# Kernel optimization log

Hardware: AMD Instinct MI355X
Metric: run time of the kernel (lower is better)

The kernel has to match this reference:

```python
import jax, jax.numpy as jnp
import numpy as np

N_IN, N_HIDDEN, N, K = 14, 256, 131072, 10

def _linear_params(key, n_in, n_out):
    kw, kb = jax.random.split(key)
    lim = 1.0 / np.sqrt(n_in)
    W = jax.random.uniform(kw, (n_in, n_out), jnp.float32, -lim, lim)
    b = jax.random.uniform(kb, (n_out,), jnp.float32, -lim, lim)
    return W, b

def setup_inputs() -> dict:
    key = jax.random.key(0)
    ks = jax.random.split(key, 8)
    towers = jax.random.normal(ks[0], (N, K, N_IN), jnp.float32)
    M1_w, M1_b = _linear_params(ks[1], N_IN + N_HIDDEN, N_HIDDEN)
    M2_w, M2_b = _linear_params(ks[2], N_HIDDEN, N_HIDDEN)
    M3_w, M3_b = _linear_params(ks[3], N_HIDDEN, N_HIDDEN)
    O1_w, O1_b = _linear_params(ks[4], N_IN + N_HIDDEN, N_HIDDEN)
    O2_w, O2_b = _linear_params(ks[5], N_HIDDEN, N_HIDDEN)
    O3_w, O3_b = _linear_params(ks[6], N_HIDDEN, 1)
    aggregate = jnp.zeros((1, N_HIDDEN), jnp.float32)
    return dict(towers=towers, aggregate=aggregate,
                M1_w=M1_w, M1_b=M1_b, M2_w=M2_w, M2_b=M2_b, M3_w=M3_w, M3_b=M3_b,
                O1_w=O1_w, O1_b=O1_b, O2_w=O2_w, O2_b=O2_b, O3_w=O3_w, O3_b=O3_b,
                k=K)

def reference(towers, aggregate,
              M1_w, M1_b, M2_w, M2_b, M3_w, M3_b,
              O1_w, O1_b, O2_w, O2_b, O3_w, O3_b, k):
    N_, K_, _ = towers.shape
    # flip along tower axis, then scan over K steps (top-down)
    tows = jnp.transpose(towers[:, ::-1, :], (1, 0, 2))  # (K, N, n_in)

    def mlp_M(x):
        h = jax.nn.relu(x @ M1_w + M1_b)
        h = jax.nn.relu(h @ M2_w + M2_b)
        return jax.nn.relu(h @ M3_w + M3_b)

    def mlp_O(x):
        h = jax.nn.relu(x @ O1_w + O1_b)
        h = jax.nn.relu(h @ O2_w + O2_b)
        return h @ O3_w + O3_b  # (N, 1)

    def step(carry, tow_k):
        summary, prod = carry
        x = jnp.concatenate([summary, tow_k], axis=1)  # (N, n_hidden + n_in)
        pred = jax.nn.sigmoid(mlp_O(x))[:, 0]
        new_summary = mlp_M(x)
        return (new_summary, prod * pred), None

    init_summary = jnp.broadcast_to(aggregate, (N_, aggregate.shape[1]))
    init_prod = jnp.ones((N_,), towers.dtype)
    (final_summary, prod), _ = jax.lax.scan(step, (init_summary, init_prod), tows)
    return prod  # (N,)
```

## Files before the change

### kernel.cpp

```cpp
#include <hip/hip_runtime.h>
#include <math.h>
#include <stdint.h>


typedef _Float16 half8 __attribute__((ext_vector_type(8)));
typedef __fp16 fp16x2 __attribute__((ext_vector_type(2)));
typedef float f32x4 __attribute__((ext_vector_type(4)));

constexpr int KS = 10;
constexpr int RSTR = 584;
constexpr float SPLIT_S = 2048.f;
constexpr float SPLIT_INV = 1.f / 2048.f;

__device__ __align__(16) _Float16 g_Wh[672 * 512];
__device__ __align__(16) _Float16 g_Wl[672 * 512];
__device__ __align__(16) uint4 g_park[2048u * 8u * 8u * 64u];

__global__ void prep_w(const float* __restrict__ O1w, const float* __restrict__ M1w,
                       const float* __restrict__ O2w, const float* __restrict__ M2w,
                       const float* __restrict__ M3w) {
  const int bid = blockIdx.x, l = threadIdx.x;
  const float* W; int Ksrc, f;
  if (bid < 144)      { W = O1w; Ksrc = 270; f = bid; }
  else if (bid < 288) { W = M1w; Ksrc = 270; f = bid - 144; }
  else if (bid < 416) { W = O2w; Ksrc = 256; f = bid - 288; }
  else if (bid < 544) { W = M2w; Ksrc = 256; f = bid - 416; }
  else                { W = M3w; Ksrc = 256; f = bid - 544; }
  const int c = f >> 4, nt = f & 15, g = l >> 4, s = l & 15;
  const int of = nt * 16 + s;
  union { half8 h; uint4 u; } hv, lv;
#pragma unroll
  for (int i = 0; i < 8; ++i) {
    const int k = c * 32 + g * 8 + i;
    const float w = (k < Ksrc) ? W[k * 256 + of] : 0.f;
    const _Float16 h = (_Float16)w;
    hv.h[i] = h;
    lv.h[i] = (_Float16)((w - (float)h) * SPLIT_S);
  }
  ((uint4*)g_Wh)[bid * 64 + l] = hv.u;
  ((uint4*)g_Wl)[bid * 64 + l] = lv.u;
}

__device__ __forceinline__ half8 as_half8(uint4 u) {
  union { uint4 u4; half8 h; } c; c.u4 = u; return c.h;
}
__device__ __forceinline__ f32x4 mfma16(half8 a, half8 b, f32x4 c) {
  return __builtin_amdgcn_mfma_f32_16x16x32_f16(a, b, c, 0, 0, 0);
}
__device__ __forceinline__ uint32_t h2bits(fp16x2 h) {
  union { fp16x2 h2; uint32_t u; } c; c.h2 = h; return c.u;
}

struct PK { uint2 hi, lo; };
__device__ __forceinline__ PK split4(float v0, float v1, float v2, float v3) {
  fp16x2 h01 = __builtin_amdgcn_cvt_pkrtz(v0, v1);
  fp16x2 h23 = __builtin_amdgcn_cvt_pkrtz(v2, v3);
  fp16x2 l01 = __builtin_amdgcn_cvt_pkrtz((v0 - (float)h01[0]) * SPLIT_S,
                                          (v1 - (float)h01[1]) * SPLIT_S);
  fp16x2 l23 = __builtin_amdgcn_cvt_pkrtz((v2 - (float)h23[0]) * SPLIT_S,
                                          (v3 - (float)h23[1]) * SPLIT_S);
  PK r;
  r.hi = make_uint2(h2bits(h01), h2bits(h23));
  r.lo = make_uint2(h2bits(l01), h2bits(l23));
  return r;
}
__device__ __forceinline__ void split1(float v, _Float16& h, _Float16& l) {
  h = (_Float16)v;
  l = (_Float16)((v - (float)h) * SPLIT_S);
}

__device__ __forceinline__ void zero24(f32x4 a1[2][4], f32x4 a2[2][4]) {
#pragma unroll
  for (int n = 0; n < 2; ++n)
#pragma unroll
    for (int sf = 0; sf < 4; ++sf) {
      a1[n][sf] = (f32x4){0.f, 0.f, 0.f, 0.f};
      a2[n][sf] = (f32x4){0.f, 0.f, 0.f, 0.f};
    }
}

template <int CHUNKS>
__device__ __forceinline__ void lgemm(f32x4 a1[2][4], f32x4 a2[2][4],
                                      const _Float16* __restrict__ Xs,
                                      const uint4* __restrict__ Wh,
                                      const uint4* __restrict__ Wl,
                                      int wu, int g, int s) {
#pragma unroll 1
  for (int c = 0; c < CHUNKS; ++c) {
    uint4 wh[2], wl[2];
#pragma unroll
    for (int n = 0; n < 2; ++n) {
      wh[n] = Wh[(c * 16 + 2 * wu + n) * 64];
      wl[n] = Wl[(c * 16 + 2 * wu + n) * 64];
    }
#pragma unroll
    for (int sf = 0; sf < 4; ++sf) {
      const _Float16* xp = Xs + (16 * sf + s) * RSTR + c * 32 + g * 8;
      half8 bh = *(const half8*)xp;
      half8 bl = *(const half8*)(xp + 288);
#pragma unroll
      for (int n = 0; n < 2; ++n) {
        a1[n][sf] = mfma16(as_half8(wh[n]), bh, a1[n][sf]);
        a2[n][sf] = mfma16(as_half8(wh[n]), bl, a2[n][sf]);
        a2[n][sf] = mfma16(as_half8(wl[n]), bh, a2[n][sf]);
      }
    }
  }
}

__device__ __forceinline__ void epi_write(const f32x4 a1[2][4], const f32x4 a2[2][4],
                                          const float* __restrict__ bias,
                                          _Float16* __restrict__ Xs,
                                          int wu, int g, int s) {
#pragma unroll
  for (int n = 0; n < 2; ++n) {
    const float4 bv = *(const float4*)(bias + (2 * wu + n) * 16 + 4 * g);
#pragma unroll
    for (int sf = 0; sf < 4; ++sf) {
      const float v0 = fmaxf(fmaf(a2[n][sf][0], SPLIT_INV, a1[n][sf][0]) + bv.x, 0.f);
      const float v1 = fmaxf(fmaf(a2[n][sf][1], SPLIT_INV, a1[n][sf][1]) + bv.y, 0.f);
      const float v2 = fmaxf(fmaf(a2[n][sf][2], SPLIT_INV, a1[n][sf][2]) + bv.z, 0.f);
      const float v3 = fmaxf(fmaf(a2[n][sf][3], SPLIT_INV, a1[n][sf][3]) + bv.w, 0.f);
      const PK p = split4(v0, v1, v2, v3);
      _Float16* yp = Xs + (16 * sf + s) * RSTR + (2 * wu + n) * 16 + 4 * g;
      *(uint2*)yp = p.hi;
      *(uint2*)(yp + 288) = p.lo;
    }
  }
}

__device__ __forceinline__ void epi_park(const f32x4 a1[2][4], const f32x4 a2[2][4],
                                         const float* __restrict__ bias,
                                         uint4* __restrict__ slot,
                                         int wu, int g, int l) {
#pragma unroll
  for (int n = 0; n < 2; ++n) {
    const float4 bv = *(const float4*)(bias + (2 * wu + n) * 16 + 4 * g);
#pragma unroll
    for (int p = 0; p < 2; ++p) {
      PK q[2];
#pragma unroll
      for (int h = 0; h < 2; ++h) {
        const int sf = 2 * p + h;
        const float v0 = fmaxf(fmaf(a2[n][sf][0], SPLIT_INV, a1[n][sf][0]) + bv.x, 0.f);
        const float v1 = fmaxf(fmaf(a2[n][sf][1], SPLIT_INV, a1[n][sf][1]) + bv.y, 0.f);
        const float v2 = fmaxf(fmaf(a2[n][sf][2], SPLIT_INV, a1[n][sf][2]) + bv.z, 0.f);
        const float v3 = fmaxf(fmaf(a2[n][sf][3], SPLIT_INV, a1[n][sf][3]) + bv.w, 0.f);
        q[h] = split4(v0, v1, v2, v3);
      }
      slot[(n * 2 + p) * 64 + l]     = make_uint4(q[0].hi.x, q[0].hi.y, q[1].hi.x, q[1].hi.y);
      slot[(4 + n * 2 + p) * 64 + l] = make_uint4(q[0].lo.x, q[0].lo.y, q[1].lo.x, q[1].lo.y);
    }
  }
}

__device__ __forceinline__ void unpark_write(const uint4 pk[8],
                                             _Float16* __restrict__ Xs,
                                             int wu, int g, int s) {
#pragma unroll
  for (int n = 0; n < 2; ++n)
#pragma unroll
    for (int p = 0; p < 2; ++p) {
      const uint4 hi = pk[n * 2 + p];
      const uint4 lo = pk[4 + n * 2 + p];
#pragma unroll
      for (int h = 0; h < 2; ++h) {
        const int sf = 2 * p + h;
        _Float16* yp = Xs + (16 * sf + s) * RSTR + (2 * wu + n) * 16 + 4 * g;
        *(uint2*)yp = h ? make_uint2(hi.z, hi.w) : make_uint2(hi.x, hi.y);
        *(uint2*)(yp + 288) = h ? make_uint2(lo.z, lo.w) : make_uint2(lo.x, lo.y);
      }
    }
}

__global__ __launch_bounds__(512, 4) void topdown_mfma(
    const float* __restrict__ towers, const float* __restrict__ aggregate,
    const float* __restrict__ O1b, const float* __restrict__ O2b,
    const float* __restrict__ O3w, const float* __restrict__ O3b,
    const float* __restrict__ M1b, const float* __restrict__ M2b,
    const float* __restrict__ M3b, float* __restrict__ out) {
  __shared__ __align__(16) _Float16 Xs[64 * RSTR];
  __shared__ __align__(16) float scr[64][8];
  const int t = threadIdx.x, l = t & 63;
  const int wu = __builtin_amdgcn_readfirstlane(t >> 6);
  const int g = l >> 4, s = l & 15;
  const int n0 = blockIdx.x * 64;
  uint4* park = g_park + ((size_t)blockIdx.x * 8 + (size_t)wu) * (8 * 64);

  for (int idx = t; idx < 64 * 288; idx += 512) {
    const int ss = idx / 288, f = idx - ss * 288;
    const float v = (f < 256) ? aggregate[f] : 0.f;
    _Float16 h, lo; split1(v, h, lo);
    Xs[ss * RSTR + f] = h;
    Xs[ss * RSTR + 288 + f] = lo;
  }

  float prod = 1.f;
  const float o3bias = O3b[0];
  f32x4 a1[2][4], a2[2][4];

  const uint4* WhL = (const uint4*)g_Wh + l;
  const uint4* WlL = (const uint4*)g_Wl + l;

  for (int kk = 0; kk < KS; ++kk) {
    const int tbase = (KS - 1 - kk) * 14;
    for (int idx = t; idx < 64 * 14; idx += 512) {
      const int ss = idx / 14, f = idx - ss * 14;
      const float v = towers[(size_t)(n0 + ss) * (KS * 14) + tbase + f];
      _Float16 h, lo; split1(v, h, lo);
      Xs[ss * RSTR + 256 + f] = h;
      Xs[ss * RSTR + 288 + 256 + f] = lo;
    }
    __syncthreads();

    zero24(a1, a2);
    lgemm<9>(a1, a2, Xs, WhL + 144 * 64, WlL + 144 * 64, wu, g, s);
    epi_park(a1, a2, M1b, park, wu, g, l);

    zero24(a1, a2);
    lgemm<9>(a1, a2, Xs, WhL, WlL, wu, g, s);
    __syncthreads();
    epi_write(a1, a2, O1b, Xs, wu, g, s);
    __syncthreads();

    zero24(a1, a2);
    lgemm<8>(a1, a2, Xs, WhL + 288 * 64, WlL + 288 * 64, wu, g, s);

    asm volatile("" ::: "memory");
    uint4 pk[8];
#pragma unroll
    for (int q = 0; q < 8; ++q) pk[q] = park[q * 64 + l];

    float tp[4] = {0.f, 0.f, 0.f, 0.f};
#pragma unroll
    for (int n = 0; n < 2; ++n) {
      const int ob = (2 * wu + n) * 16 + 4 * g;
      const float4 bv = *(const float4*)(O2b + ob);
      const float4 ov = *(const float4*)(O3w + ob);
      const float bb[4] = {bv.x, bv.y, bv.z, bv.w};
      const float oo[4] = {ov.x, ov.y, ov.z, ov.w};
#pragma unroll
      for (int sf = 0; sf < 4; ++sf)
#pragma unroll
        for (int r = 0; r < 4; ++r)
          tp[sf] += fmaxf(fmaf(a2[n][sf][r], SPLIT_INV, a1[n][sf][r]) + bb[r], 0.f) * oo[r];
    }
#pragma unroll
    for (int sf = 0; sf < 4; ++sf) {
      tp[sf] += __shfl_xor(tp[sf], 16);
      tp[sf] += __shfl_xor(tp[sf], 32);
    }
    if (g == 0) {
#pragma unroll
      for (int sf = 0; sf < 4; ++sf) scr[16 * sf + s][wu] = tp[sf];
    }
    __syncthreads();

    unpark_write(pk, Xs, wu, g, s);
    if (t < 64) {
      const float4 s0 = *(const float4*)(scr[t]);
      const float4 s1 = *(const float4*)(scr[t] + 4);
      const float tt = ((s0.x + s0.y) + (s0.z + s0.w)) +
                       ((s1.x + s1.y) + (s1.z + s1.w)) + o3bias;
      prod *= 1.f / (1.f + expf(-tt));
    }
    __syncthreads();

    zero24(a1, a2);
    lgemm<8>(a1, a2, Xs, WhL + 416 * 64, WlL + 416 * 64, wu, g, s);
    __syncthreads();
    epi_write(a1, a2, M2b, Xs, wu, g, s);
    __syncthreads();

    zero24(a1, a2);
    lgemm<8>(a1, a2, Xs, WhL + 544 * 64, WlL + 544 * 64, wu, g, s);
    __syncthreads();
    epi_write(a1, a2, M3b, Xs, wu, g, s);
  }

  if (t < 64) out[n0 + t] = prod;
}

extern "C" void kernel_launch(void* const* d_in, const int* in_sizes, int n_in,
                              void* d_out, int out_size, void* d_ws, size_t ws_size,
                              hipStream_t stream) {
  const float* towers    = (const float*)d_in[0];
  const float* aggregate = (const float*)d_in[1];
  const float* M1w = (const float*)d_in[2];
  const float* M1b = (const float*)d_in[3];
  const float* M2w = (const float*)d_in[4];
  const float* M2b = (const float*)d_in[5];
  const float* M3w = (const float*)d_in[6];
  const float* M3b = (const float*)d_in[7];
  const float* O1w = (const float*)d_in[8];
  const float* O1b = (const float*)d_in[9];
  const float* O2w = (const float*)d_in[10];
  const float* O2b = (const float*)d_in[11];
  const float* O3w = (const float*)d_in[12];
  const float* O3b = (const float*)d_in[13];
  float* out = (float*)d_out;

  prep_w<<<672, 64, 0, stream>>>(O1w, M1w, O2w, M2w, M3w);

  const int nblocks = out_size / 64;
  topdown_mfma<<<nblocks, 512, 0, stream>>>(towers, aggregate, O1b, O2b, O3w,
                                            O3b, M1b, M2b, M3b, out);
}
```

Before: 2.408 ms.

## Retile warp work to 4 output tiles by 2 sample tiles

Each wave's GEMM tile changes from 2 output-column fragments by 4 sample fragments to 4 output-column fragments by 2 sample fragments, splitting the 8 waves into 4 column groups and 2 sample groups. Each wave now loads twice as many weight fragments from global/L2 per chunk but half as many activation fragments from LDS. The O3 reduction scratch shrinks to 4 partials per sample. The intent is to cut LDS read traffic per MFMA, at the cost of doubling the per-wave weight fetches from global memory.

After: 2.853 ms. +18.5%, slower.

```diff
diff --git a/kernel.cpp b/kernel.cpp
--- a/kernel.cpp
+++ b/kernel.cpp
@@ -69,37 +69,38 @@
   l = (_Float16)((v - (float)h) * SPLIT_S);
 }
 
-__device__ __forceinline__ void zero24(f32x4 a1[2][4], f32x4 a2[2][4]) {
-#pragma unroll
-  for (int n = 0; n < 2; ++n)
-#pragma unroll
-    for (int sf = 0; sf < 4; ++sf) {
+__device__ __forceinline__ void zero42(f32x4 a1[4][2], f32x4 a2[4][2]) {
+#pragma unroll
+  for (int n = 0; n < 4; ++n)
+#pragma unroll
+    for (int sf = 0; sf < 2; ++sf) {
       a1[n][sf] = (f32x4){0.f, 0.f, 0.f, 0.f};
       a2[n][sf] = (f32x4){0.f, 0.f, 0.f, 0.f};
     }
 }
 
 template <int CHUNKS>
-__device__ __forceinline__ void lgemm(f32x4 a1[2][4], f32x4 a2[2][4],
+__device__ __forceinline__ void lgemm(f32x4 a1[4][2], f32x4 a2[4][2],
                                       const _Float16* __restrict__ Xs,
                                       const uint4* __restrict__ Wh,
                                       const uint4* __restrict__ Wl,
-                                      int wu, int g, int s) {
+                                      int wn, int sg, int g, int s) {
 #pragma unroll 1
   for (int c = 0; c < CHUNKS; ++c) {
-    uint4 wh[2], wl[2];
-#pragma unroll
-    for (int n = 0; n < 2; ++n) {
-      wh[n] = Wh[(c * 16 + 2 * wu + n) * 64];
-      wl[n] = Wl[(c * 16 + 2 * wu + n) * 64];
-    }
-#pragma unroll
-    for (int sf = 0; sf < 4; ++sf) {
-      const _Float16* xp = Xs + (16 * sf + s) * RSTR + c * 32 + g * 8;
+    uint4 wh[4], wl[4];
+#pragma unroll
+    for (int n = 0; n < 4; ++n) {
+      wh[n] = Wh[(c * 16 + 4 * wn + n) * 64];
+      wl[n] = Wl[(c * 16 + 4 * wn + n) * 64];
+    }
+#pragma unroll
+    for (int sf = 0; sf < 2; ++sf) {
+      const _Float16* xp =
+          Xs + (16 * (2 * sg + sf) + s) * RSTR + c * 32 + g * 8;
       half8 bh = *(const half8*)xp;
       half8 bl = *(const half8*)(xp + 288);
 #pragma unroll
-      for (int n = 0; n < 2; ++n) {
+      for (int n = 0; n < 4; ++n) {
         a1[n][sf] = mfma16(as_half8(wh[n]), bh, a1[n][sf]);
         a2[n][sf] = mfma16(as_half8(wh[n]), bl, a2[n][sf]);
         a2[n][sf] = mfma16(as_half8(wl[n]), bh, a2[n][sf]);
@@ -108,69 +109,64 @@
   }
 }
 
-__device__ __forceinline__ void epi_write(const f32x4 a1[2][4], const f32x4 a2[2][4],
+__device__ __forceinline__ void epi_write(const f32x4 a1[4][2], const f32x4 a2[4][2],
                                           const float* __restrict__ bias,
                                           _Float16* __restrict__ Xs,
-                                          int wu, int g, int s) {
-#pragma unroll
-  for (int n = 0; n < 2; ++n) {
-    const float4 bv = *(const float4*)(bias + (2 * wu + n) * 16 + 4 * g);
-#pragma unroll
-    for (int sf = 0; sf < 4; ++sf) {
+                                          int wn, int sg, int g, int s) {
+#pragma unroll
+  for (int n = 0; n < 4; ++n) {
+    const float4 bv = *(const float4*)(bias + (4 * wn + n) * 16 + 4 * g);
+#pragma unroll
+    for (int sf = 0; sf < 2; ++sf) {
       const float v0 = fmaxf(fmaf(a2[n][sf][0], SPLIT_INV, a1[n][sf][0]) + bv.x, 0.f);
       const float v1 = fmaxf(fmaf(a2[n][sf][1], SPLIT_INV, a1[n][sf][1]) + bv.y, 0.f);
       const float v2 = fmaxf(fmaf(a2[n][sf][2], SPLIT_INV, a1[n][sf][2]) + bv.z, 0.f);
       const float v3 = fmaxf(fmaf(a2[n][sf][3], SPLIT_INV, a1[n][sf][3]) + bv.w, 0.f);
       const PK p = split4(v0, v1, v2, v3);
-      _Float16* yp = Xs + (16 * sf + s) * RSTR + (2 * wu + n) * 16 + 4 * g;
+      _Float16* yp =
+          Xs + (16 * (2 * sg + sf) + s) * RSTR + (4 * wn + n) * 16 + 4 * g;
       *(uint2*)yp = p.hi;
       *(uint2*)(yp + 288) = p.lo;
     }
   }
 }
 
-__device__ __forceinline__ void epi_park(const f32x4 a1[2][4], const f32x4 a2[2][4],
+__device__ __forceinline__ void epi_park(const f32x4 a1[4][2], const f32x4 a2[4][2],
                                          const float* __restrict__ bias,
                                          uint4* __restrict__ slot,
-                                         int wu, int g, int l) {
-#pragma unroll
-  for (int n = 0; n < 2; ++n) {
-    const float4 bv = *(const float4*)(bias + (2 * wu + n) * 16 + 4 * g);
-#pragma unroll
-    for (int p = 0; p < 2; ++p) {
-      PK q[2];
-#pragma unroll
-      for (int h = 0; h < 2; ++h) {
-        const int sf = 2 * p + h;
-        const float v0 = fmaxf(fmaf(a2[n][sf][0], SPLIT_INV, a1[n][sf][0]) + bv.x, 0.f);
-        const float v1 = fmaxf(fmaf(a2[n][sf][1], SPLIT_INV, a1[n][sf][1]) + bv.y, 0.f);
-        const float v2 = fmaxf(fmaf(a2[n][sf][2], SPLIT_INV, a1[n][sf][2]) + bv.z, 0.f);
-        const float v3 = fmaxf(fmaf(a2[n][sf][3], SPLIT_INV, a1[n][sf][3]) + bv.w, 0.f);
-        q[h] = split4(v0, v1, v2, v3);
-      }
-      slot[(n * 2 + p) * 64 + l]     = make_uint4(q[0].hi.x, q[0].hi.y, q[1].hi.x, q[1].hi.y);
-      slot[(4 + n * 2 + p) * 64 + l] = make_uint4(q[0].lo.x, q[0].lo.y, q[1].lo.x, q[1].lo.y);
-    }
+                                         int wn, int g, int l) {
+#pragma unroll
+  for (int n = 0; n < 4; ++n) {
+    const float4 bv = *(const float4*)(bias + (4 * wn + n) * 16 + 4 * g);
+    PK q[2];
+#pragma unroll
+    for (int sf = 0; sf < 2; ++sf) {
+      const float v0 = fmaxf(fmaf(a2[n][sf][0], SPLIT_INV, a1[n][sf][0]) + bv.x, 0.f);
+      const float v1 = fmaxf(fmaf(a2[n][sf][1], SPLIT_INV, a1[n][sf][1]) + bv.y, 0.f);
+      const float v2 = fmaxf(fmaf(a2[n][sf][2], SPLIT_INV, a1[n][sf][2]) + bv.z, 0.f);
+      const float v3 = fmaxf(fmaf(a2[n][sf][3], SPLIT_INV, a1[n][sf][3]) + bv.w, 0.f);
+      q[sf] = split4(v0, v1, v2, v3);
+    }
+    slot[n * 64 + l]       = make_uint4(q[0].hi.x, q[0].hi.y, q[1].hi.x, q[1].hi.y);
+    slot[(4 + n) * 64 + l] = make_uint4(q[0].lo.x, q[0].lo.y, q[1].lo.x, q[1].lo.y);
   }
 }
 
 __device__ __forceinline__ void unpark_write(const uint4 pk[8],
                                              _Float16* __restrict__ Xs,
-                                             int wu, int g, int s) {
-#pragma unroll
-  for (int n = 0; n < 2; ++n)
-#pragma unroll
-    for (int p = 0; p < 2; ++p) {
-      const uint4 hi = pk[n * 2 + p];
-      const uint4 lo = pk[4 + n * 2 + p];
-#pragma unroll
-      for (int h = 0; h < 2; ++h) {
-        const int sf = 2 * p + h;
-        _Float16* yp = Xs + (16 * sf + s) * RSTR + (2 * wu + n) * 16 + 4 * g;
-        *(uint2*)yp = h ? make_uint2(hi.z, hi.w) : make_uint2(hi.x, hi.y);
-        *(uint2*)(yp + 288) = h ? make_uint2(lo.z, lo.w) : make_uint2(lo.x, lo.y);
-      }
-    }
+                                             int wn, int sg, int g, int s) {
+#pragma unroll
+  for (int n = 0; n < 4; ++n) {
+    const uint4 hi = pk[n];
+    const uint4 lo = pk[4 + n];
+#pragma unroll
+    for (int sf = 0; sf < 2; ++sf) {
+      _Float16* yp =
+          Xs + (16 * (2 * sg + sf) + s) * RSTR + (4 * wn + n) * 16 + 4 * g;
+      *(uint2*)yp = sf ? make_uint2(hi.z, hi.w) : make_uint2(hi.x, hi.y);
+      *(uint2*)(yp + 288) = sf ? make_uint2(lo.z, lo.w) : make_uint2(lo.x, lo.y);
+    }
+  }
 }
 
 __global__ __launch_bounds__(512, 4) void topdown_mfma(
@@ -180,9 +176,11 @@
     const float* __restrict__ M1b, const float* __restrict__ M2b,
     const float* __restrict__ M3b, float* __restrict__ out) {
   __shared__ __align__(16) _Float16 Xs[64 * RSTR];
-  __shared__ __align__(16) float scr[64][8];
+  __shared__ __align__(16) float scr[64][4];
   const int t = threadIdx.x, l = t & 63;
   const int wu = __builtin_amdgcn_readfirstlane(t >> 6);
+  const int wn = wu & 3;
+  const int sg = wu >> 2;
   const int g = l >> 4, s = l & 15;
   const int n0 = blockIdx.x * 64;
   uint4* park = g_park + ((size_t)blockIdx.x * 8 + (size_t)wu) * (8 * 64);
@@ -197,7 +195,7 @@
 
   float prod = 1.f;
   const float o3bias = O3b[0];
-  f32x4 a1[2][4], a2[2][4];
+  f32x4 a1[4][2], a2[4][2];
 
   const uint4* WhL = (const uint4*)g_Wh + l;
   const uint4* WlL = (const uint4*)g_Wl + l;
@@ -213,69 +211,66 @@
     }
     __syncthreads();
 
-    zero24(a1, a2);
-    lgemm<9>(a1, a2, Xs, WhL + 144 * 64, WlL + 144 * 64, wu, g, s);
-    epi_park(a1, a2, M1b, park, wu, g, l);
-
-    zero24(a1, a2);
-    lgemm<9>(a1, a2, Xs, WhL, WlL, wu, g, s);
-    __syncthreads();
-    epi_write(a1, a2, O1b, Xs, wu, g, s);
-    __syncthreads();
-
-    zero24(a1, a2);
-    lgemm<8>(a1, a2, Xs, WhL + 288 * 64, WlL + 288 * 64, wu, g, s);
+    zero42(a1, a2);
+    lgemm<9>(a1, a2, Xs, WhL + 144 * 64, WlL + 144 * 64, wn, sg, g, s);
+    epi_park(a1, a2, M1b, park, wn, g, l);
+
+    zero42(a1, a2);
+    lgemm<9>(a1, a2, Xs, WhL, WlL, wn, sg, g, s);
+    __syncthreads();
+    epi_write(a1, a2, O1b, Xs, wn, sg, g, s);
+    __syncthreads();
+
+    zero42(a1, a2);
+    lgemm<8>(a1, a2, Xs, WhL + 288 * 64, WlL + 288 * 64, wn, sg, g, s);
 
     asm volatile("" ::: "memory");
     uint4 pk[8];
 #pragma unroll
     for (int q = 0; q < 8; ++q) pk[q] = park[q * 64 + l];
 
-    float tp[4] = {0.f, 0.f, 0.f, 0.f};
-#pragma unroll
-    for (int n = 0; n < 2; ++n) {
-      const int ob = (2 * wu + n) * 16 + 4 * g;
+    float tp[2] = {0.f, 0.f};
+#pragma unroll
+    for (int n = 0; n < 4; ++n) {
+      const int ob = (4 * wn + n) * 16 + 4 * g;
       const float4 bv = *(const float4*)(O2b + ob);
       const float4 ov = *(const float4*)(O3w + ob);
       const float bb[4] = {bv.x, bv.y, bv.z, bv.w};
       const float oo[4] = {ov.x, ov.y, ov.z, ov.w};
 #pragma unroll
-      for (int sf = 0; sf < 4; ++sf)
+      for (int sf = 0; sf < 2; ++sf)
 #pragma unroll
         for (int r = 0; r < 4; ++r)
           tp[sf] += fmaxf(fmaf(a2[n][sf][r], SPLIT_INV, a1[n][sf][r]) + bb[r], 0.f) * oo[r];
     }
 #pragma unroll
-    for (int sf = 0; sf < 4; ++sf) {
+    for (int sf = 0; sf < 2; ++sf) {
       tp[sf] += __shfl_xor(tp[sf], 16);
       tp[sf] += __shfl_xor(tp[sf], 32);
     }
     if (g == 0) {
 #pragma unroll
-      for (int sf = 0; sf < 4; ++sf) scr[16 * sf + s][wu] = tp[sf];
-    }
-    __syncthreads();
-
-    unpark_write(pk, Xs, wu, g, s);
+      for (int sf = 0; sf < 2; ++sf) scr[16 * (2 * sg + sf) + s][wn] = tp[sf];
+    }
+    __syncthreads();
+
+    unpark_write(pk, Xs, wn, sg, g, s);
     if (t < 64) {
-      const float4 s0 = *(const float4*)(scr[t]);
-      const float4 s1 = *(const float4*)(scr[t] + 4);
-      const float tt = ((s0.x + s0.y) + (s0.z + s0.w)) +
-                       ((s1.x + s1.y) + (s1.z + s1.w)) + o3bias;
-      prod *= 1.f / (1.f + expf(-tt));
-    }
-    __syncthreads();
-
-    zero24(a1, a2);
-    lgemm<8>(a1, a2, Xs, WhL + 416 * 64, WlL + 416 * 64, wu, g, s);
-    __syncthreads();
-    epi_write(a1, a2, M2b, Xs, wu, g, s);
-    __syncthreads();
-
-    zero24(a1, a2);
-    lgemm<8>(a1, a2, Xs, WhL + 544 * 64, WlL + 544 * 64, wu, g, s);
-    __syncthreads();
-    epi_write(a1, a2, M3b, Xs, wu, g, s);
+      const float4 sv = *(const float4*)(scr[t]);
+      prod *= 1.f / (1.f + expf(-(sv.x + sv.y + sv.z + sv.w + o3bias)));
+    }
+    __syncthreads();
+
+    zero42(a1, a2);
+    lgemm<8>(a1, a2, Xs, WhL + 416 * 64, WlL + 416 * 64, wn, sg, g, s);
+    __syncthreads();
+    epi_write(a1, a2, M2b, Xs, wn, sg, g, s);
+    __syncthreads();
+
+    zero42(a1, a2);
+    lgemm<8>(a1, a2, Xs, WhL + 544 * 64, WlL + 544 * 64, wn, sg, g, s);
+    __syncthreads();
+    epi_write(a1, a2, M3b, Xs, wn, sg, g, s);
   }
 
   if (t < 64) out[n0 + t] = prod;
```

## Switch split-fp16 GEMMs from 16x16x32 to 32x32x16 MFMA with weight prefetch

Applied to the files above, without the earlier changes.

Replaces the 16x16x32 MFMA tiling with 32x32x16 MFMA tiles, so each wave computes 32 output features by 64 samples in two 16-wide accumulators. The weight prep layout, epilogues, parking and the O3 reduction are rewritten to match the new accumulator layout. The GEMM loop also double-buffers weight loads across chunks. The aim is fewer LDS reads of X per MFMA and better MFMA throughput, at the cost of larger accumulator register use, which risks occupancy under the 512x4 launch bounds.

Measured after the change: 3.078 ms. 27.8% more time.

```diff
diff --git a/kernel.cpp b/kernel.cpp
--- a/kernel.cpp
+++ b/kernel.cpp
@@ -5,7 +5,7 @@
 
 typedef _Float16 half8 __attribute__((ext_vector_type(8)));
 typedef __fp16 fp16x2 __attribute__((ext_vector_type(2)));
-typedef float f32x4 __attribute__((ext_vector_type(4)));
+typedef float f32x16 __attribute__((ext_vector_type(16)));
 
 constexpr int KS = 10;
 constexpr int RSTR = 584;
@@ -26,12 +26,13 @@
   else if (bid < 416) { W = O2w; Ksrc = 256; f = bid - 288; }
   else if (bid < 544) { W = M2w; Ksrc = 256; f = bid - 416; }
   else                { W = M3w; Ksrc = 256; f = bid - 544; }
-  const int c = f >> 4, nt = f & 15, g = l >> 4, s = l & 15;
-  const int of = nt * 16 + s;
+  const int kc = f >> 3, ot = f & 7;
+  const int of = ot * 32 + (l & 31);
+  const int kb = kc * 16 + (l >> 5) * 8;
   union { half8 h; uint4 u; } hv, lv;
 #pragma unroll
   for (int i = 0; i < 8; ++i) {
-    const int k = c * 32 + g * 8 + i;
+    const int k = kb + i;
     const float w = (k < Ksrc) ? W[k * 256 + of] : 0.f;
     const _Float16 h = (_Float16)w;
     hv.h[i] = h;
@@ -44,8 +45,8 @@
 __device__ __forceinline__ half8 as_half8(uint4 u) {
   union { uint4 u4; half8 h; } c; c.u4 = u; return c.h;
 }
-__device__ __forceinline__ f32x4 mfma16(half8 a, half8 b, f32x4 c) {
-  return __builtin_amdgcn_mfma_f32_16x16x32_f16(a, b, c, 0, 0, 0);
+__device__ __forceinline__ f32x16 mfma32(half8 a, half8 b, f32x16 c) {
+  return __builtin_amdgcn_mfma_f32_32x32x16_f16(a, b, c, 0, 0, 0);
 }
 __device__ __forceinline__ uint32_t h2bits(fp16x2 h) {
   union { fp16x2 h2; uint32_t u; } c; c.h2 = h; return c.u;
@@ -69,108 +70,129 @@
   l = (_Float16)((v - (float)h) * SPLIT_S);
 }
 
-__device__ __forceinline__ void zero24(f32x4 a1[2][4], f32x4 a2[2][4]) {
-#pragma unroll
-  for (int n = 0; n < 2; ++n)
-#pragma unroll
-    for (int sf = 0; sf < 4; ++sf) {
-      a1[n][sf] = (f32x4){0.f, 0.f, 0.f, 0.f};
-      a2[n][sf] = (f32x4){0.f, 0.f, 0.f, 0.f};
-    }
+struct W4 { uint4 h0, l0, h1, l1; };
+__device__ __forceinline__ W4 ldw(const uint4* __restrict__ Wh,
+                                  const uint4* __restrict__ Wl, int fb) {
+  W4 w;
+  w.h0 = Wh[fb * 64];
+  w.l0 = Wl[fb * 64];
+  w.h1 = Wh[(fb + 8) * 64];
+  w.l1 = Wl[(fb + 8) * 64];
+  return w;
+}
+
+__device__ __forceinline__ void body32(f32x16& a10, f32x16& a11,
+                                       f32x16& a20, f32x16& a21,
+                                       const _Float16* __restrict__ Xp0,
+                                       const _Float16* __restrict__ Xp1,
+                                       int coff, const W4& w) {
+#pragma unroll
+  for (int kk = 0; kk < 2; ++kk) {
+    const half8 wh = as_half8(kk ? w.h1 : w.h0);
+    const half8 wl = as_half8(kk ? w.l1 : w.l0);
+    const int o = coff + kk * 16;
+    half8 bh0 = *(const half8*)(Xp0 + o);
+    half8 bl0 = *(const half8*)(Xp0 + o + 288);
+    a10 = mfma32(wh, bh0, a10);
+    a20 = mfma32(wh, bl0, a20);
+    a20 = mfma32(wl, bh0, a20);
+    half8 bh1 = *(const half8*)(Xp1 + o);
+    half8 bl1 = *(const half8*)(Xp1 + o + 288);
+    a11 = mfma32(wh, bh1, a11);
+    a21 = mfma32(wh, bl1, a21);
+    a21 = mfma32(wl, bh1, a21);
+  }
 }
 
 template <int CHUNKS>
-__device__ __forceinline__ void lgemm(f32x4 a1[2][4], f32x4 a2[2][4],
-                                      const _Float16* __restrict__ Xs,
-                                      const uint4* __restrict__ Wh,
-                                      const uint4* __restrict__ Wl,
-                                      int wu, int g, int s) {
+__device__ __forceinline__ void lgemm32(f32x16& a10, f32x16& a11,
+                                        f32x16& a20, f32x16& a21,
+                                        const _Float16* __restrict__ Xp0,
+                                        const _Float16* __restrict__ Xp1,
+                                        const uint4* __restrict__ Wh,
+                                        const uint4* __restrict__ Wl, int wu) {
+  W4 A = ldw(Wh, Wl, wu);
+  W4 B;
 #pragma unroll 1
-  for (int c = 0; c < CHUNKS; ++c) {
-    uint4 wh[2], wl[2];
-#pragma unroll
-    for (int n = 0; n < 2; ++n) {
-      wh[n] = Wh[(c * 16 + 2 * wu + n) * 64];
-      wl[n] = Wl[(c * 16 + 2 * wu + n) * 64];
-    }
-#pragma unroll
-    for (int sf = 0; sf < 4; ++sf) {
-      const _Float16* xp = Xs + (16 * sf + s) * RSTR + c * 32 + g * 8;
-      half8 bh = *(const half8*)xp;
-      half8 bl = *(const half8*)(xp + 288);
-#pragma unroll
-      for (int n = 0; n < 2; ++n) {
-        a1[n][sf] = mfma16(as_half8(wh[n]), bh, a1[n][sf]);
-        a2[n][sf] = mfma16(as_half8(wh[n]), bl, a2[n][sf]);
-        a2[n][sf] = mfma16(as_half8(wl[n]), bh, a2[n][sf]);
-      }
-    }
-  }
-}
-
-__device__ __forceinline__ void epi_write(const f32x4 a1[2][4], const f32x4 a2[2][4],
+  for (int c = 0; c + 2 <= CHUNKS; c += 2) {
+    B = ldw(Wh, Wl, 16 * (c + 1) + wu);
+    body32(a10, a11, a20, a21, Xp0, Xp1, c * 32, A);
+    if (c + 2 < CHUNKS) A = ldw(Wh, Wl, 16 * (c + 2) + wu);
+    body32(a10, a11, a20, a21, Xp0, Xp1, (c + 1) * 32, B);
+  }
+  if (CHUNKS & 1) body32(a10, a11, a20, a21, Xp0, Xp1, (CHUNKS - 1) * 32, A);
+}
+
+__device__ __forceinline__ void zero2(f32x16& a, f32x16& b) {
+#pragma unroll
+  for (int i = 0; i < 16; ++i) { a[i] = 0.f; b[i] = 0.f; }
+}
+
+__device__ __forceinline__ void epi_write(const f32x16 a1[2], const f32x16 a2[2],
                                           const float* __restrict__ bias,
                                           _Float16* __restrict__ Xs,
-                                          int wu, int g, int s) {
-#pragma unroll
-  for (int n = 0; n < 2; ++n) {
-    const float4 bv = *(const float4*)(bias + (2 * wu + n) * 16 + 4 * g);
-#pragma unroll
-    for (int sf = 0; sf < 4; ++sf) {
-      const float v0 = fmaxf(fmaf(a2[n][sf][0], SPLIT_INV, a1[n][sf][0]) + bv.x, 0.f);
-      const float v1 = fmaxf(fmaf(a2[n][sf][1], SPLIT_INV, a1[n][sf][1]) + bv.y, 0.f);
-      const float v2 = fmaxf(fmaf(a2[n][sf][2], SPLIT_INV, a1[n][sf][2]) + bv.z, 0.f);
-      const float v3 = fmaxf(fmaf(a2[n][sf][3], SPLIT_INV, a1[n][sf][3]) + bv.w, 0.f);
+                                          int wu, int col, int hi) {
+#pragma unroll
+  for (int sf = 0; sf < 2; ++sf) {
+    _Float16* yrow = Xs + (32 * sf + col) * RSTR;
+#pragma unroll
+    for (int q = 0; q < 4; ++q) {
+      const int ofb = 32 * wu + 8 * q + 4 * hi;
+      const float4 bv = *(const float4*)(bias + ofb);
+      const float v0 = fmaxf(fmaf(a2[sf][4*q+0], SPLIT_INV, a1[sf][4*q+0]) + bv.x, 0.f);
+      const float v1 = fmaxf(fmaf(a2[sf][4*q+1], SPLIT_INV, a1[sf][4*q+1]) + bv.y, 0.f);
+      const float v2 = fmaxf(fmaf(a2[sf][4*q+2], SPLIT_INV, a1[sf][4*q+2]) + bv.z, 0.f);
+      const float v3 = fmaxf(fmaf(a2[sf][4*q+3], SPLIT_INV, a1[sf][4*q+3]) + bv.w, 0.f);
       const PK p = split4(v0, v1, v2, v3);
-      _Float16* yp = Xs + (16 * sf + s) * RSTR + (2 * wu + n) * 16 + 4 * g;
-      *(uint2*)yp = p.hi;
-      *(uint2*)(yp + 288) = p.lo;
-    }
-  }
-}
-
-__device__ __forceinline__ void epi_park(const f32x4 a1[2][4], const f32x4 a2[2][4],
+      *(uint2*)(yrow + ofb) = p.hi;
+      *(uint2*)(yrow + 288 + ofb) = p.lo;
+    }
+  }
+}
+
+__device__ __forceinline__ void epi_park(const f32x16 a1[2], const f32x16 a2[2],
                                          const float* __restrict__ bias,
                                          uint4* __restrict__ slot,
-                                         int wu, int g, int l) {
-#pragma unroll
-  for (int n = 0; n < 2; ++n) {
-    const float4 bv = *(const float4*)(bias + (2 * wu + n) * 16 + 4 * g);
-#pragma unroll
-    for (int p = 0; p < 2; ++p) {
-      PK q[2];
+                                         int wu, int hi, int l) {
+#pragma unroll
+  for (int sf = 0; sf < 2; ++sf)
+#pragma unroll
+    for (int qq = 0; qq < 2; ++qq) {
+      PK p[2];
 #pragma unroll
       for (int h = 0; h < 2; ++h) {
-        const int sf = 2 * p + h;
-        const float v0 = fmaxf(fmaf(a2[n][sf][0], SPLIT_INV, a1[n][sf][0]) + bv.x, 0.f);
-        const float v1 = fmaxf(fmaf(a2[n][sf][1], SPLIT_INV, a1[n][sf][1]) + bv.y, 0.f);
-        const float v2 = fmaxf(fmaf(a2[n][sf][2], SPLIT_INV, a1[n][sf][2]) + bv.z, 0.f);
-        const float v3 = fmaxf(fmaf(a2[n][sf][3], SPLIT_INV, a1[n][sf][3]) + bv.w, 0.f);
-        q[h] = split4(v0, v1, v2, v3);
+        const int q = 2 * qq + h;
+        const int ofb = 32 * wu + 8 * q + 4 * hi;
+        const float4 bv = *(const float4*)(bias + ofb);
+        const float v0 = fmaxf(fmaf(a2[sf][4*q+0], SPLIT_INV, a1[sf][4*q+0]) + bv.x, 0.f);
+        const float v1 = fmaxf(fmaf(a2[sf][4*q+1], SPLIT_INV, a1[sf][4*q+1]) + bv.y, 0.f);
+        const float v2 = fmaxf(fmaf(a2[sf][4*q+2], SPLIT_INV, a1[sf][4*q+2]) + bv.z, 0.f);
+        const float v3 = fmaxf(fmaf(a2[sf][4*q+3], SPLIT_INV, a1[sf][4*q+3]) + bv.w, 0.f);
+        p[h] = split4(v0, v1, v2, v3);
       }
-      slot[(n * 2 + p) * 64 + l]     = make_uint4(q[0].hi.x, q[0].hi.y, q[1].hi.x, q[1].hi.y);
-      slot[(4 + n * 2 + p) * 64 + l] = make_uint4(q[0].lo.x, q[0].lo.y, q[1].lo.x, q[1].lo.y);
-    }
-  }
+      slot[(sf * 2 + qq) * 64 + l]     = make_uint4(p[0].hi.x, p[0].hi.y, p[1].hi.x, p[1].hi.y);
+      slot[(4 + sf * 2 + qq) * 64 + l] = make_uint4(p[0].lo.x, p[0].lo.y, p[1].lo.x, p[1].lo.y);
+    }
 }
 
 __device__ __forceinline__ void unpark_write(const uint4 pk[8],
                                              _Float16* __restrict__ Xs,
-                                             int wu, int g, int s) {
-#pragma unroll
-  for (int n = 0; n < 2; ++n)
-#pragma unroll
-    for (int p = 0; p < 2; ++p) {
-      const uint4 hi = pk[n * 2 + p];
-      const uint4 lo = pk[4 + n * 2 + p];
-#pragma unroll
-      for (int h = 0; h < 2; ++h) {
-        const int sf = 2 * p + h;
-        _Float16* yp = Xs + (16 * sf + s) * RSTR + (2 * wu + n) * 16 + 4 * g;
-        *(uint2*)yp = h ? make_uint2(hi.z, hi.w) : make_uint2(hi.x, hi.y);
-        *(uint2*)(yp + 288) = h ? make_uint2(lo.z, lo.w) : make_uint2(lo.x, lo.y);
-      }
-    }
+                                             int wu, int col, int hi) {
+#pragma unroll
+  for (int sf = 0; sf < 2; ++sf) {
+    _Float16* yrow = Xs + (32 * sf + col) * RSTR;
+#pragma unroll
+    for (int qq = 0; qq < 2; ++qq) {
+      const uint4 h4 = pk[sf * 2 + qq];
+      const uint4 l4 = pk[4 + sf * 2 + qq];
+      const int ofb0 = 32 * wu + 8 * (2 * qq) + 4 * hi;
+      const int ofb1 = ofb0 + 8;
+      *(uint2*)(yrow + ofb0) = make_uint2(h4.x, h4.y);
+      *(uint2*)(yrow + 288 + ofb0) = make_uint2(l4.x, l4.y);
+      *(uint2*)(yrow + ofb1) = make_uint2(h4.z, h4.w);
+      *(uint2*)(yrow + 288 + ofb1) = make_uint2(l4.z, l4.w);
+    }
+  }
 }
 
 __global__ __launch_bounds__(512, 4) void topdown_mfma(
@@ -183,9 +205,12 @@
   __shared__ __align__(16) float scr[64][8];
   const int t = threadIdx.x, l = t & 63;
   const int wu = __builtin_amdgcn_readfirstlane(t >> 6);
-  const int g = l >> 4, s = l & 15;
+  const int col = l & 31, hi = l >> 5;
   const int n0 = blockIdx.x * 64;
   uint4* park = g_park + ((size_t)blockIdx.x * 8 + (size_t)wu) * (8 * 64);
+
+  const _Float16* Xp0 = Xs + col * RSTR + hi * 8;
+  const _Float16* Xp1 = Xs + (32 + col) * RSTR + hi * 8;
 
   for (int idx = t; idx < 64 * 288; idx += 512) {
     const int ss = idx / 288, f = idx - ss * 288;
@@ -197,7 +222,7 @@
 
   float prod = 1.f;
   const float o3bias = O3b[0];
-  f32x4 a1[2][4], a2[2][4];
+  f32x16 a1[2], a2[2];
 
   const uint4* WhL = (const uint4*)g_Wh + l;
   const uint4* WlL = (const uint4*)g_Wl + l;
@@ -213,50 +238,46 @@
     }
     __syncthreads();
 
-    zero24(a1, a2);
-    lgemm<9>(a1, a2, Xs, WhL + 144 * 64, WlL + 144 * 64, wu, g, s);
-    epi_park(a1, a2, M1b, park, wu, g, l);
-
-    zero24(a1, a2);
-    lgemm<9>(a1, a2, Xs, WhL, WlL, wu, g, s);
-    __syncthreads();
-    epi_write(a1, a2, O1b, Xs, wu, g, s);
-    __syncthreads();
-
-    zero24(a1, a2);
-    lgemm<8>(a1, a2, Xs, WhL + 288 * 64, WlL + 288 * 64, wu, g, s);
+    zero2(a1[0], a2[0]); zero2(a1[1], a2[1]);
+    lgemm32<9>(a1[0], a1[1], a2[0], a2[1], Xp0, Xp1, WhL + 144 * 64, WlL + 144 * 64, wu);
+    epi_park(a1, a2, M1b, park, wu, hi, l);
+
+    zero2(a1[0], a2[0]); zero2(a1[1], a2[1]);
+    lgemm32<9>(a1[0], a1[1], a2[0], a2[1], Xp0, Xp1, WhL, WlL, wu);
+    __syncthreads();
+    epi_write(a1, a2, O1b, Xs, wu, col, hi);
+    __syncthreads();
+
+    zero2(a1[0], a2[0]); zero2(a1[1], a2[1]);
+    lgemm32<8>(a1[0], a1[1], a2[0], a2[1], Xp0, Xp1, WhL + 288 * 64, WlL + 288 * 64, wu);
 
     asm volatile("" ::: "memory");
     uint4 pk[8];
 #pragma unroll
     for (int q = 0; q < 8; ++q) pk[q] = park[q * 64 + l];
 
-    float tp[4] = {0.f, 0.f, 0.f, 0.f};
-#pragma unroll
-    for (int n = 0; n < 2; ++n) {
-      const int ob = (2 * wu + n) * 16 + 4 * g;
-      const float4 bv = *(const float4*)(O2b + ob);
-      const float4 ov = *(const float4*)(O3w + ob);
-      const float bb[4] = {bv.x, bv.y, bv.z, bv.w};
-      const float oo[4] = {ov.x, ov.y, ov.z, ov.w};
-#pragma unroll
-      for (int sf = 0; sf < 4; ++sf)
-#pragma unroll
-        for (int r = 0; r < 4; ++r)
-          tp[sf] += fmaxf(fmaf(a2[n][sf][r], SPLIT_INV, a1[n][sf][r]) + bb[r], 0.f) * oo[r];
-    }
-#pragma unroll
-    for (int sf = 0; sf < 4; ++sf) {
-      tp[sf] += __shfl_xor(tp[sf], 16);
-      tp[sf] += __shfl_xor(tp[sf], 32);
-    }
-    if (g == 0) {
-#pragma unroll
-      for (int sf = 0; sf < 4; ++sf) scr[16 * sf + s][wu] = tp[sf];
-    }
-    __syncthreads();
-
-    unpark_write(pk, Xs, wu, g, s);
+    float tp[2] = {0.f, 0.f};
+#pragma unroll
+    for (int sf = 0; sf < 2; ++sf)
+#pragma unroll
+      for (int q = 0; q < 4; ++q) {
+        const int ofb = 32 * wu + 8 * q + 4 * hi;
+        const float4 bv = *(const float4*)(O2b + ofb);
+        const float4 ov = *(const float4*)(O3w + ofb);
+        tp[sf] += fmaxf(fmaf(a2[sf][4*q+0], SPLIT_INV, a1[sf][4*q+0]) + bv.x, 0.f) * ov.x;
+        tp[sf] += fmaxf(fmaf(a2[sf][4*q+1], SPLIT_INV, a1[sf][4*q+1]) + bv.y, 0.f) * ov.y;
+        tp[sf] += fmaxf(fmaf(a2[sf][4*q+2], SPLIT_INV, a1[sf][4*q+2]) + bv.z, 0.f) * ov.z;
+        tp[sf] += fmaxf(fmaf(a2[sf][4*q+3], SPLIT_INV, a1[sf][4*q+3]) + bv.w, 0.f) * ov.w;
+      }
+    tp[0] += __shfl_xor(tp[0], 32);
+    tp[1] += __shfl_xor(tp[1], 32);
+    if (hi == 0) {
+      scr[col][wu] = tp[0];
+      scr[32 + col][wu] = tp[1];
+    }
+    __syncthreads();
+
+    unpark_write(pk, Xs, wu, col, hi);
     if (t < 64) {
       const float4 s0 = *(const float4*)(scr[t]);
       const float4 s1 = *(const float4*)(scr[t] + 4);
@@ -266,16 +287,16 @@
     }
     __syncthreads();
 
-    zero24(a1, a2);
-    lgemm<8>(a1, a2, Xs, WhL + 416 * 64, WlL + 416 * 64, wu, g, s);
-    __syncthreads();
-    epi_write(a1, a2, M2b, Xs, wu, g, s);
-    __syncthreads();
-
-    zero24(a1, a2);
-    lgemm<8>(a1, a2, Xs, WhL + 544 * 64, WlL + 544 * 64, wu, g, s);
-    __syncthreads();
-    epi_write(a1, a2, M3b, Xs, wu, g, s);
+    zero2(a1[0], a2[0]); zero2(a1[1], a2[1]);
+    lgemm32<8>(a1[0], a1[1], a2[0], a2[1], Xp0, Xp1, WhL + 416 * 64, WlL + 416 * 64, wu);
+    __syncthreads();
+    epi_write(a1, a2, M2b, Xs, wu, col, hi);
+    __syncthreads();
+
+    zero2(a1[0], a2[0]); zero2(a1[1], a2[1]);
+    lgemm32<8>(a1[0], a1[1], a2[0], a2[1], Xp0, Xp1, WhL + 544 * 64, WlL + 544 * 64, wu);
+    __syncthreads();
+    epi_write(a1, a2, M3b, Xs, wu, col, hi);
   }
 
   if (t < 64) out[n0 + t] = prod;
```

## Halve rows per block to 32 and software-pipeline weight loads in GEMM loop

Applied to the files above, without the earlier changes.

Each block now handles 32 rows instead of 64, halving the shared activation buffer, the accumulator registers and the park slots, and doubling the block count. The GEMM loop is restructured to double-buffer the global weight fragments across chunks, so the next chunk's weights are prefetched while the current chunk's MFMAs run. This aims to raise occupancy and hide weight-load latency. The cost is that each weight fragment loaded from global memory now feeds half as many rows, doubling total weight traffic per output.

Result: slower. 3.275 ms (+36.0%).

```diff
diff --git a/kernel.cpp b/kernel.cpp
--- a/kernel.cpp
+++ b/kernel.cpp
@@ -14,7 +14,7 @@
 
 __device__ __align__(16) _Float16 g_Wh[672 * 512];
 __device__ __align__(16) _Float16 g_Wl[672 * 512];
-__device__ __align__(16) uint4 g_park[2048u * 8u * 8u * 64u];
+__device__ __align__(16) uint4 g_park[4096u * 8u * 4u * 64u];
 
 __global__ void prep_w(const float* __restrict__ O1w, const float* __restrict__ M1w,
                        const float* __restrict__ O2w, const float* __restrict__ M2w,
@@ -69,46 +69,75 @@
   l = (_Float16)((v - (float)h) * SPLIT_S);
 }
 
-__device__ __forceinline__ void zero24(f32x4 a1[2][4], f32x4 a2[2][4]) {
+struct W2 { uint4 h0, h1, l0, l1; };
+__device__ __forceinline__ W2 ldw2(const uint4* __restrict__ Wh,
+                                   const uint4* __restrict__ Wl, int fb) {
+  W2 w;
+  w.h0 = Wh[fb * 64];
+  w.h1 = Wh[(fb + 1) * 64];
+  w.l0 = Wl[fb * 64];
+  w.l1 = Wl[(fb + 1) * 64];
+  return w;
+}
+
+__device__ __forceinline__ void body(f32x4 a1[2][2], f32x4 a2[2][2],
+                                     const W2& w,
+                                     const _Float16* __restrict__ Xp0,
+                                     const _Float16* __restrict__ Xp1,
+                                     int coff) {
+  const half8 wh0 = as_half8(w.h0), wh1 = as_half8(w.h1);
+  const half8 wl0 = as_half8(w.l0), wl1 = as_half8(w.l1);
+  {
+    half8 bh = *(const half8*)(Xp0 + coff);
+    half8 bl = *(const half8*)(Xp0 + coff + 288);
+    a1[0][0] = mfma16(wh0, bh, a1[0][0]);
+    a2[0][0] = mfma16(wh0, bl, a2[0][0]);
+    a2[0][0] = mfma16(wl0, bh, a2[0][0]);
+    a1[1][0] = mfma16(wh1, bh, a1[1][0]);
+    a2[1][0] = mfma16(wh1, bl, a2[1][0]);
+    a2[1][0] = mfma16(wl1, bh, a2[1][0]);
+  }
+  {
+    half8 bh = *(const half8*)(Xp1 + coff);
+    half8 bl = *(const half8*)(Xp1 + coff + 288);
+    a1[0][1] = mfma16(wh0, bh, a1[0][1]);
+    a2[0][1] = mfma16(wh0, bl, a2[0][1]);
+    a2[0][1] = mfma16(wl0, bh, a2[0][1]);
+    a1[1][1] = mfma16(wh1, bh, a1[1][1]);
+    a2[1][1] = mfma16(wh1, bl, a2[1][1]);
+    a2[1][1] = mfma16(wl1, bh, a2[1][1]);
+  }
+}
+
+template <int CHUNKS>
+__device__ __forceinline__ void lgemm(f32x4 a1[2][2], f32x4 a2[2][2],
+                                      const _Float16* __restrict__ Xp0,
+                                      const _Float16* __restrict__ Xp1,
+                                      const uint4* __restrict__ Wh,
+                                      const uint4* __restrict__ Wl, int wu) {
+  W2 A = ldw2(Wh, Wl, 2 * wu);
+  W2 B;
+#pragma unroll 1
+  for (int c = 0; c + 2 <= CHUNKS; c += 2) {
+    B = ldw2(Wh, Wl, 16 * (c + 1) + 2 * wu);
+    body(a1, a2, A, Xp0, Xp1, c * 32);
+    if (c + 2 < CHUNKS) A = ldw2(Wh, Wl, 16 * (c + 2) + 2 * wu);
+    body(a1, a2, B, Xp0, Xp1, (c + 1) * 32);
+  }
+  if (CHUNKS & 1) body(a1, a2, A, Xp0, Xp1, (CHUNKS - 1) * 32);
+}
+
+__device__ __forceinline__ void zero22(f32x4 a1[2][2], f32x4 a2[2][2]) {
 #pragma unroll
   for (int n = 0; n < 2; ++n)
 #pragma unroll
-    for (int sf = 0; sf < 4; ++sf) {
+    for (int sf = 0; sf < 2; ++sf) {
       a1[n][sf] = (f32x4){0.f, 0.f, 0.f, 0.f};
       a2[n][sf] = (f32x4){0.f, 0.f, 0.f, 0.f};
     }
 }
 
-template <int CHUNKS>
-__device__ __forceinline__ void lgemm(f32x4 a1[2][4], f32x4 a2[2][4],
-                                      const _Float16* __restrict__ Xs,
-                                      const uint4* __restrict__ Wh,
-                                      const uint4* __restrict__ Wl,
-                                      int wu, int g, int s) {
-#pragma unroll 1
-  for (int c = 0; c < CHUNKS; ++c) {
-    uint4 wh[2], wl[2];
-#pragma unroll
-    for (int n = 0; n < 2; ++n) {
-      wh[n] = Wh[(c * 16 + 2 * wu + n) * 64];
-      wl[n] = Wl[(c * 16 + 2 * wu + n) * 64];
-    }
-#pragma unroll
-    for (int sf = 0; sf < 4; ++sf) {
-      const _Float16* xp = Xs + (16 * sf + s) * RSTR + c * 32 + g * 8;
-      half8 bh = *(const half8*)xp;
-      half8 bl = *(const half8*)(xp + 288);
-#pragma unroll
-      for (int n = 0; n < 2; ++n) {
-        a1[n][sf] = mfma16(as_half8(wh[n]), bh, a1[n][sf]);
-        a2[n][sf] = mfma16(as_half8(wh[n]), bl, a2[n][sf]);
-        a2[n][sf] = mfma16(as_half8(wl[n]), bh, a2[n][sf]);
-      }
-    }
-  }
-}
-
-__device__ __forceinline__ void epi_write(const f32x4 a1[2][4], const f32x4 a2[2][4],
+__device__ __forceinline__ void epi_write(const f32x4 a1[2][2], const f32x4 a2[2][2],
                                           const float* __restrict__ bias,
                                           _Float16* __restrict__ Xs,
                                           int wu, int g, int s) {
@@ -116,7 +145,7 @@
   for (int n = 0; n < 2; ++n) {
     const float4 bv = *(const float4*)(bias + (2 * wu + n) * 16 + 4 * g);
 #pragma unroll
-    for (int sf = 0; sf < 4; ++sf) {
+    for (int sf = 0; sf < 2; ++sf) {
       const float v0 = fmaxf(fmaf(a2[n][sf][0], SPLIT_INV, a1[n][sf][0]) + bv.x, 0.f);
       const float v1 = fmaxf(fmaf(a2[n][sf][1], SPLIT_INV, a1[n][sf][1]) + bv.y, 0.f);
       const float v2 = fmaxf(fmaf(a2[n][sf][2], SPLIT_INV, a1[n][sf][2]) + bv.z, 0.f);
@@ -129,48 +158,41 @@
   }
 }
 
-__device__ __forceinline__ void epi_park(const f32x4 a1[2][4], const f32x4 a2[2][4],
+__device__ __forceinline__ void epi_park(const f32x4 a1[2][2], const f32x4 a2[2][2],
                                          const float* __restrict__ bias,
                                          uint4* __restrict__ slot,
                                          int wu, int g, int l) {
 #pragma unroll
   for (int n = 0; n < 2; ++n) {
     const float4 bv = *(const float4*)(bias + (2 * wu + n) * 16 + 4 * g);
-#pragma unroll
-    for (int p = 0; p < 2; ++p) {
-      PK q[2];
-#pragma unroll
-      for (int h = 0; h < 2; ++h) {
-        const int sf = 2 * p + h;
-        const float v0 = fmaxf(fmaf(a2[n][sf][0], SPLIT_INV, a1[n][sf][0]) + bv.x, 0.f);
-        const float v1 = fmaxf(fmaf(a2[n][sf][1], SPLIT_INV, a1[n][sf][1]) + bv.y, 0.f);
-        const float v2 = fmaxf(fmaf(a2[n][sf][2], SPLIT_INV, a1[n][sf][2]) + bv.z, 0.f);
-        const float v3 = fmaxf(fmaf(a2[n][sf][3], SPLIT_INV, a1[n][sf][3]) + bv.w, 0.f);
-        q[h] = split4(v0, v1, v2, v3);
-      }
-      slot[(n * 2 + p) * 64 + l]     = make_uint4(q[0].hi.x, q[0].hi.y, q[1].hi.x, q[1].hi.y);
-      slot[(4 + n * 2 + p) * 64 + l] = make_uint4(q[0].lo.x, q[0].lo.y, q[1].lo.x, q[1].lo.y);
-    }
-  }
-}
-
-__device__ __forceinline__ void unpark_write(const uint4 pk[8],
+    PK q[2];
+#pragma unroll
+    for (int sf = 0; sf < 2; ++sf) {
+      const float v0 = fmaxf(fmaf(a2[n][sf][0], SPLIT_INV, a1[n][sf][0]) + bv.x, 0.f);
+      const float v1 = fmaxf(fmaf(a2[n][sf][1], SPLIT_INV, a1[n][sf][1]) + bv.y, 0.f);
+      const float v2 = fmaxf(fmaf(a2[n][sf][2], SPLIT_INV, a1[n][sf][2]) + bv.z, 0.f);
+      const float v3 = fmaxf(fmaf(a2[n][sf][3], SPLIT_INV, a1[n][sf][3]) + bv.w, 0.f);
+      q[sf] = split4(v0, v1, v2, v3);
+    }
+    slot[n * 64 + l]       = make_uint4(q[0].hi.x, q[0].hi.y, q[1].hi.x, q[1].hi.y);
+    slot[(2 + n) * 64 + l] = make_uint4(q[0].lo.x, q[0].lo.y, q[1].lo.x, q[1].lo.y);
+  }
+}
+
+__device__ __forceinline__ void unpark_write(const uint4 pk[4],
                                              _Float16* __restrict__ Xs,
                                              int wu, int g, int s) {
 #pragma unroll
-  for (int n = 0; n < 2; ++n)
-#pragma unroll
-    for (int p = 0; p < 2; ++p) {
-      const uint4 hi = pk[n * 2 + p];
-      const uint4 lo = pk[4 + n * 2 + p];
-#pragma unroll
-      for (int h = 0; h < 2; ++h) {
-        const int sf = 2 * p + h;
-        _Float16* yp = Xs + (16 * sf + s) * RSTR + (2 * wu + n) * 16 + 4 * g;
-        *(uint2*)yp = h ? make_uint2(hi.z, hi.w) : make_uint2(hi.x, hi.y);
-        *(uint2*)(yp + 288) = h ? make_uint2(lo.z, lo.w) : make_uint2(lo.x, lo.y);
-      }
-    }
+  for (int n = 0; n < 2; ++n) {
+    const uint4 hi = pk[n];
+    const uint4 lo = pk[2 + n];
+#pragma unroll
+    for (int sf = 0; sf < 2; ++sf) {
+      _Float16* yp = Xs + (16 * sf + s) * RSTR + (2 * wu + n) * 16 + 4 * g;
+      *(uint2*)yp = sf ? make_uint2(hi.z, hi.w) : make_uint2(hi.x, hi.y);
+      *(uint2*)(yp + 288) = sf ? make_uint2(lo.z, lo.w) : make_uint2(lo.x, lo.y);
+    }
+  }
 }
 
 __global__ __launch_bounds__(512, 4) void topdown_mfma(
@@ -179,15 +201,18 @@
     const float* __restrict__ O3w, const float* __restrict__ O3b,
     const float* __restrict__ M1b, const float* __restrict__ M2b,
     const float* __restrict__ M3b, float* __restrict__ out) {
-  __shared__ __align__(16) _Float16 Xs[64 * RSTR];
-  __shared__ __align__(16) float scr[64][8];
+  __shared__ __align__(16) _Float16 Xs[32 * RSTR];
+  __shared__ __align__(16) float scr[32][8];
   const int t = threadIdx.x, l = t & 63;
   const int wu = __builtin_amdgcn_readfirstlane(t >> 6);
   const int g = l >> 4, s = l & 15;
-  const int n0 = blockIdx.x * 64;
-  uint4* park = g_park + ((size_t)blockIdx.x * 8 + (size_t)wu) * (8 * 64);
-
-  for (int idx = t; idx < 64 * 288; idx += 512) {
+  const int n0 = blockIdx.x * 32;
+  uint4* park = g_park + ((size_t)blockIdx.x * 8 + (size_t)wu) * (4 * 64);
+
+  const _Float16* Xp0 = Xs + s * RSTR + g * 8;
+  const _Float16* Xp1 = Xs + (16 + s) * RSTR + g * 8;
+
+  for (int idx = t; idx < 32 * 288; idx += 512) {
     const int ss = idx / 288, f = idx - ss * 288;
     const float v = (f < 256) ? aggregate[f] : 0.f;
     _Float16 h, lo; split1(v, h, lo);
@@ -197,15 +222,15 @@
 
   float prod = 1.f;
   const float o3bias = O3b[0];
-  f32x4 a1[2][4], a2[2][4];
+  f32x4 a1[2][2], a2[2][2];
 
   const uint4* WhL = (const uint4*)g_Wh + l;
   const uint4* WlL = (const uint4*)g_Wl + l;
 
   for (int kk = 0; kk < KS; ++kk) {
     const int tbase = (KS - 1 - kk) * 14;
-    for (int idx = t; idx < 64 * 14; idx += 512) {
-      const int ss = idx / 14, f = idx - ss * 14;
+    if (t < 448) {
+      const int ss = t / 14, f = t - ss * 14;
       const float v = towers[(size_t)(n0 + ss) * (KS * 14) + tbase + f];
       _Float16 h, lo; split1(v, h, lo);
       Xs[ss * RSTR + 256 + f] = h;
@@ -213,25 +238,25 @@
     }
     __syncthreads();
 
-    zero24(a1, a2);
-    lgemm<9>(a1, a2, Xs, WhL + 144 * 64, WlL + 144 * 64, wu, g, s);
+    zero22(a1, a2);
+    lgemm<9>(a1, a2, Xp0, Xp1, WhL + 144 * 64, WlL + 144 * 64, wu);
     epi_park(a1, a2, M1b, park, wu, g, l);
 
-    zero24(a1, a2);
-    lgemm<9>(a1, a2, Xs, WhL, WlL, wu, g, s);
+    zero22(a1, a2);
+    lgemm<9>(a1, a2, Xp0, Xp1, WhL, WlL, wu);
     __syncthreads();
     epi_write(a1, a2, O1b, Xs, wu, g, s);
     __syncthreads();
 
-    zero24(a1, a2);
-    lgemm<8>(a1, a2, Xs, WhL + 288 * 64, WlL + 288 * 64, wu, g, s);
+    zero22(a1, a2);
+    lgemm<8>(a1, a2, Xp0, Xp1, WhL + 288 * 64, WlL + 288 * 64, wu);
 
     asm volatile("" ::: "memory");
-    uint4 pk[8];
-#pragma unroll
-    for (int q = 0; q < 8; ++q) pk[q] = park[q * 64 + l];
-
-    float tp[4] = {0.f, 0.f, 0.f, 0.f};
+    uint4 pk[4];
+#pragma unroll
+    for (int q = 0; q < 4; ++q) pk[q] = park[q * 64 + l];
+
+    float tp[2] = {0.f, 0.f};
 #pragma unroll
     for (int n = 0; n < 2; ++n) {
       const int ob = (2 * wu + n) * 16 + 4 * g;
@@ -240,24 +265,24 @@
       const float bb[4] = {bv.x, bv.y, bv.z, bv.w};
       const float oo[4] = {ov.x, ov.y, ov.z, ov.w};
 #pragma unroll
-      for (int sf = 0; sf < 4; ++sf)
+      for (int sf = 0; sf < 2; ++sf)
 #pragma unroll
         for (int r = 0; r < 4; ++r)
           tp[sf] += fmaxf(fmaf(a2[n][sf][r], SPLIT_INV, a1[n][sf][r]) + bb[r], 0.f) * oo[r];
     }
 #pragma unroll
-    for (int sf = 0; sf < 4; ++sf) {
+    for (int sf = 0; sf < 2; ++sf) {
       tp[sf] += __shfl_xor(tp[sf], 16);
       tp[sf] += __shfl_xor(tp[sf], 32);
     }
     if (g == 0) {
-#pragma unroll
-      for (int sf = 0; sf < 4; ++sf) scr[16 * sf + s][wu] = tp[sf];
+      scr[s][wu] = tp[0];
+      scr[16 + s][wu] = tp[1];
     }
     __syncthreads();
 
     unpark_write(pk, Xs, wu, g, s);
-    if (t < 64) {
+    if (t < 32) {
       const float4 s0 = *(const float4*)(scr[t]);
       const float4 s1 = *(const float4*)(scr[t] + 4);
       const float tt = ((s0.x + s0.y) + (s0.z + s0.w)) +
@@ -266,19 +291,19 @@
     }
     __syncthreads();
 
-    zero24(a1, a2);
-    lgemm<8>(a1, a2, Xs, WhL + 416 * 64, WlL + 416 * 64, wu, g, s);
+    zero22(a1, a2);
+    lgemm<8>(a1, a2, Xp0, Xp1, WhL + 416 * 64, WlL + 416 * 64, wu);
     __syncthreads();
     epi_write(a1, a2, M2b, Xs, wu, g, s);
     __syncthreads();
 
-    zero24(a1, a2);
-    lgemm<8>(a1, a2, Xs, WhL + 544 * 64, WlL + 544 * 64, wu, g, s);
+    zero22(a1, a2);
+    lgemm<8>(a1, a2, Xp0, Xp1, WhL + 544 * 64, WlL + 544 * 64, wu);
     __syncthreads();
     epi_write(a1, a2, M3b, Xs, wu, g, s);
   }
 
-  if (t < 64) out[n0 + t] = prod;
+  if (t < 32) out[n0 + t] = prod;
 }
 
 extern "C" void kernel_launch(void* const* d_in, const int* in_sizes, int n_in,
@@ -302,7 +327,7 @@
 
   prep_w<<<672, 64, 0, stream>>>(O1w, M1w, O2w, M2w, M3w);
 
-  const int nblocks = out_size / 64;
+  const int nblocks = out_size / 32;
   topdown_mfma<<<nblocks, 512, 0, stream>>>(towers, aggregate, O1b, O2b, O3w,
                                             O3b, M1b, M2b, M3b, out);
 }
```
